# Optimization experiments

Measured on AMD Instinct MI355X. Metric: run time of the kernel, lower is better.

Reference implementation:

```python
import jax, jax.numpy as jnp
import numpy as np

B, S, H, K = 64, 512, 768, 21  # batch, seq_len, bert hidden, num_labels


def setup_inputs() -> dict:
    key = jax.random.key(0)
    ks = jax.random.split(key, 8)
    hidden = jax.random.normal(ks[0], (B, S, H), jnp.float32)  # post-BERT states
    W = jax.random.normal(ks[1], (H, K), jnp.float32) * 0.02    # classifier weight
    b = jnp.zeros((K,), jnp.float32)                            # classifier bias
    start_transitions = jax.random.uniform(ks[2], (K,), jnp.float32, -0.1, 0.1)
    transitions = jax.random.uniform(ks[3], (K, K), jnp.float32, -0.1, 0.1)
    end_transitions = jax.random.uniform(ks[4], (K,), jnp.float32, -0.1, 0.1)
    labels = jax.random.randint(ks[5], (B, S), 0, K)
    # torchcrf requires mask[:, 0] == 1; use variable-length prefix masks
    lengths = jax.random.randint(ks[6], (B,), S // 2, S + 1)
    attention_mask = jnp.arange(S)[None, :] < lengths[:, None]  # [B,S] bool
    return dict(hidden=hidden, W=W, b=b,
                start_transitions=start_transitions,
                transitions=transitions,
                end_transitions=end_transitions,
                labels=labels, attention_mask=attention_mask)


def _crf_nll(logits, labels, mask, start_t, trans, end_t):
    """torchcrf CRF forward (reduction='sum' log-likelihood), negated."""
    fmask = mask.astype(logits.dtype)  # [B,S]
    # ---- numerator: score of the gold path ----
    emit = jnp.take_along_axis(logits, labels[..., None], axis=2)[..., 0]  # [B,S]
    tr = trans[labels[:, :-1], labels[:, 1:]]                              # [B,S-1]
    num = start_t[labels[:, 0]] + emit[:, 0] \
        + jnp.sum((emit[:, 1:] + tr) * fmask[:, 1:], axis=1)
    lengths = mask.sum(axis=1)
    last_tags = jnp.take_along_axis(labels, (lengths - 1)[:, None], axis=1)[:, 0]
    num = num + end_t[last_tags]
    # ---- denominator: forward algorithm (logsumexp recurrence) ----
    alpha0 = start_t[None, :] + logits[:, 0]           # [B,K]
    ems = jnp.swapaxes(logits[:, 1:], 0, 1)            # [S-1,B,K]
    ms = jnp.swapaxes(mask[:, 1:], 0, 1)               # [S-1,B]

    def step(alpha, xs):
        em, m = xs
        nxt = jax.scipy.special.logsumexp(
            alpha[:, :, None] + trans[None, :, :] + em[:, None, :], axis=1)
        return jnp.where(m[:, None], nxt, alpha), None

    alpha, _ = jax.lax.scan(step, alpha0, (ems, ms))
    logZ = jax.scipy.special.logsumexp(alpha + end_t[None, :], axis=1)  # [B]
    return jnp.sum(logZ - num)  # negative log-likelihood (sum over batch)


def reference(hidden, W, b, start_transitions, transitions, end_transitions,
              labels, attention_mask):
    # dropout is identity in eval; the GRU in __init__ is unused in forward
    logits = hidden @ W + b  # [B,S,K]
    nll = _crf_nll(logits, labels, attention_mask,
                   start_transitions, transitions, end_transitions)
    # module returns (logits, -1 * log_likelihood) = (logits, nll)
    return (logits, nll)
```

## Files before the change

### kernel.cpp

```cpp
#include <hip/hip_runtime.h>

#define BSZ 64
#define SEQ 512
#define HID 768
#define NK  21

#define REP21(X) X(0) X(1) X(2) X(3) X(4) X(5) X(6) X(7) X(8) X(9) X(10) \
                 X(11) X(12) X(13) X(14) X(15) X(16) X(17) X(18) X(19) X(20)

__global__ __launch_bounds__(256) void gemm_bias_kernel(
    const float* __restrict__ hidden, const float* __restrict__ W,
    const float* __restrict__ bias, float* __restrict__ out)
{
    __shared__ float hs[128 * 65];
    __shared__ float part[4][64 * NK];

    const int tid  = threadIdx.x;
    const int lane = tid & 63;
    const int wv   = __builtin_amdgcn_readfirstlane(tid >> 6);
    const int cw   = tid & 31;
    const int rr   = tid >> 5;

    const float* gbase = hidden + (size_t)blockIdx.x * 64 * HID;

#define DECL(i) float a##i = 0.f;
    REP21(DECL)
#undef DECL

    for (int ch = 0; ch < 6; ++ch) {
        __syncthreads();
        const float* gsrc = gbase + ch * 128;
        #pragma unroll
        for (int sub = 0; sub < 4; ++sub) {
            const int col = sub * 32 + cw;
            #pragma unroll
            for (int p = 0; p < 8; ++p) {
                const int row = p * 8 + rr;
                hs[col * 65 + row] = gsrc[(size_t)row * HID + col];
            }
        }
        __syncthreads();

        const float* wb   = W + (size_t)(ch * 128 + wv * 32) * NK;
        const float* hcol = hs + (size_t)(wv * 32) * 65 + lane;
        #pragma unroll 4
        for (int cc = 0; cc < 32; ++cc) {
            const float h = hcol[cc * 65];
            const float* w = wb + cc * NK;
#define STEP(i) a##i = fmaf(h, w[i], a##i);
            REP21(STEP)
#undef STEP
        }
    }

    float* pp = &part[wv][lane * NK];
#define ST(i) pp[i] = a##i;
    REP21(ST)
#undef ST
    __syncthreads();

    const int base_out = blockIdx.x * (64 * NK);
    for (int idx = tid; idx < 64 * NK; idx += 256) {
        const int k = idx - (idx / NK) * NK;
        const float s = part[0][idx] + part[1][idx] + part[2][idx] + part[3][idx];
        out[base_out + idx] = s + bias[k];
    }
}

__global__ __launch_bounds__(128) void crf_kernel(
    const float* __restrict__ logits,
    const float* __restrict__ start_t,
    const float* __restrict__ trans,
    const float* __restrict__ end_t,
    const int* __restrict__ labels,
    const int* __restrict__ mask,
    float* __restrict__ per_batch)
{
    __shared__ __align__(16) float Xl[SEQ * NK];
    __shared__ float C[SEQ];
    __shared__ float comb[24];

    const int b    = blockIdx.x;
    const int tid  = threadIdx.x;
    const int lane = tid & 63;
    const int wid  = tid >> 6;

    {
        const float4* g4 = (const float4*)(logits + (size_t)b * SEQ * NK);
        float4* l4 = (float4*)Xl;
        for (int idx = tid; idx < SEQ * NK / 4; idx += 128) l4[idx] = g4[idx];
    }

    const int* lab = labels + b * SEQ;
    const int* msk = mask   + b * SEQ;

    int cnt = 0;
    for (int t = lane; t < SEQ; t += 64) cnt += (msk[t] != 0);
    #pragma unroll
    for (int off = 32; off > 0; off >>= 1) cnt += __shfl_xor(cnt, off, 64);
    const int L = cnt;
    const int m = L >> 1;

    __syncthreads();

    {
        float numacc = 0.f;
        for (int t = tid; t < L; t += 128) {
            if (t == 0) numacc += start_t[lab[0]] + Xl[lab[0]];
            else        numacc += Xl[t * NK + lab[t]] + trans[lab[t - 1] * NK + lab[t]];
        }
        if (tid == 0) numacc += end_t[lab[L - 1]];
        #pragma unroll
        for (int off = 32; off > 0; off >>= 1) numacc += __shfl_xor(numacc, off, 64);
        if (lane == 0) comb[22 + wid] = numacc;
    }

    for (int t = tid; t < SEQ; t += 128) C[t] = Xl[t * NK];
    __syncthreads();

    for (int idx = tid; idx < SEQ * NK; idx += 128) {
        const int t = idx / NK;
        Xl[idx] = __expf(Xl[idx] - C[t]);
    }
    __syncthreads();

    const int jj = (lane < NK) ? lane : NK - 1;

#define RL(v, k) __uint_as_float(__builtin_amdgcn_readlane(__float_as_uint(v), k))

    float a;
    float Orenorm = 0.f;
    float csum = 0.f;

    if (wid == 0) {
        float Ecol[NK];
        #pragma unroll
        for (int k = 0; k < NK; ++k) Ecol[k] = __expf(trans[k * NK + jj]);

        a = __expf(start_t[jj]) * Xl[jj];
        for (int t = lane; t <= m; t += 64) csum += C[t];

        float xv = Xl[NK + jj];
        float xn = Xl[2 * NK + jj];
        for (int t = 1; t <= m; ++t) {
            const float xn2 = Xl[(t + 2) * NK + jj];
            float s0 = RL(a, 0) * Ecol[0];
            float s1 = RL(a, 1) * Ecol[1];
            float s2 = RL(a, 2) * Ecol[2];
            s0 = fmaf(RL(a,  3), Ecol[ 3], s0);
            s1 = fmaf(RL(a,  4), Ecol[ 4], s1);
            s2 = fmaf(RL(a,  5), Ecol[ 5], s2);
            s0 = fmaf(RL(a,  6), Ecol[ 6], s0);
            s1 = fmaf(RL(a,  7), Ecol[ 7], s1);
            s2 = fmaf(RL(a,  8), Ecol[ 8], s2);
            s0 = fmaf(RL(a,  9), Ecol[ 9], s0);
            s1 = fmaf(RL(a, 10), Ecol[10], s1);
            s2 = fmaf(RL(a, 11), Ecol[11], s2);
            s0 = fmaf(RL(a, 12), Ecol[12], s0);
            s1 = fmaf(RL(a, 13), Ecol[13], s1);
            s2 = fmaf(RL(a, 14), Ecol[14], s2);
            s0 = fmaf(RL(a, 15), Ecol[15], s0);
            s1 = fmaf(RL(a, 16), Ecol[16], s1);
            s2 = fmaf(RL(a, 17), Ecol[17], s2);
            s0 = fmaf(RL(a, 18), Ecol[18], s0);
            s1 = fmaf(RL(a, 19), Ecol[19], s1);
            s2 = fmaf(RL(a, 20), Ecol[20], s2);
            a = ((s0 + s1) + s2) * xv;
            if ((t & 7) == 0) {
                const float mm = __uint_as_float(
                    __builtin_amdgcn_readfirstlane(__float_as_uint(a)));
                a *= __builtin_amdgcn_rcpf(mm);
                Orenorm += __logf(mm);
            }
            xv = xn; xn = xn2;
        }
    } else {
        float Erow[NK];
        #pragma unroll
        for (int k = 0; k < NK; ++k) Erow[k] = __expf(trans[jj * NK + k]);

        a = __expf(end_t[jj]);
        for (int t = m + 1 + lane; t < L; t += 64) csum += C[t];

        float xv = Xl[(L - 1) * NK + jj];
        float xn = Xl[max(L - 2, 0) * NK + jj];
        for (int t = L - 1; t > m; --t) {
            const float xn2 = Xl[max(t - 2, 0) * NK + jj];
            const float u = a * xv;
            float s0 = RL(u, 0) * Erow[0];
            float s1 = RL(u, 1) * Erow[1];
            float s2 = RL(u, 2) * Erow[2];
            s0 = fmaf(RL(u,  3), Erow[ 3], s0);
            s1 = fmaf(RL(u,  4), Erow[ 4], s1);
            s2 = fmaf(RL(u,  5), Erow[ 5], s2);
            s0 = fmaf(RL(u,  6), Erow[ 6], s0);
            s1 = fmaf(RL(u,  7), Erow[ 7], s1);
            s2 = fmaf(RL(u,  8), Erow[ 8], s2);
            s0 = fmaf(RL(u,  9), Erow[ 9], s0);
            s1 = fmaf(RL(u, 10), Erow[10], s1);
            s2 = fmaf(RL(u, 11), Erow[11], s2);
            s0 = fmaf(RL(u, 12), Erow[12], s0);
            s1 = fmaf(RL(u, 13), Erow[13], s1);
            s2 = fmaf(RL(u, 14), Erow[14], s2);
            s0 = fmaf(RL(u, 15), Erow[15], s0);
            s1 = fmaf(RL(u, 16), Erow[16], s1);
            s2 = fmaf(RL(u, 17), Erow[17], s2);
            s0 = fmaf(RL(u, 18), Erow[18], s0);
            s1 = fmaf(RL(u, 19), Erow[19], s1);
            s2 = fmaf(RL(u, 20), Erow[20], s2);
            a = (s0 + s1) + s2;
            if ((t & 7) == 0) {
                const float mm = __uint_as_float(
                    __builtin_amdgcn_readfirstlane(__float_as_uint(a)));
                a *= __builtin_amdgcn_rcpf(mm);
                Orenorm += __logf(mm);
            }
            xv = xn; xn = xn2;
        }
    }
#undef RL

    #pragma unroll
    for (int off = 32; off > 0; off >>= 1) csum += __shfl_xor(csum, off, 64);

    if (wid == 1) {
        if (lane < NK) comb[lane] = a;
        if (lane == 0) comb[21] = csum + Orenorm;
    }
    __syncthreads();

    if (wid == 0) {
        float val = (lane < NK) ? a * comb[lane] : 0.f;
        #pragma unroll
        for (int off = 32; off > 0; off >>= 1) val += __shfl_xor(val, off, 64);
        if (lane == 0) {
            const float OF  = csum + Orenorm;
            const float num = comb[22] + comb[23];
            per_batch[b] = OF + comb[21] + __logf(val) - num;
        }
    }
}

__global__ __launch_bounds__(64) void reduce_kernel(
    const float* __restrict__ pb, float* __restrict__ out)
{
    float v = pb[threadIdx.x];
    #pragma unroll
    for (int off = 32; off > 0; off >>= 1) v += __shfl_xor(v, off, 64);
    if (threadIdx.x == 0) out[BSZ * SEQ * NK] = v;
}

extern "C" void kernel_launch(void* const* d_in, const int* in_sizes, int n_in,
                              void* d_out, int out_size, void* d_ws, size_t ws_size,
                              hipStream_t stream)
{
    const float* hidden  = (const float*)d_in[0];
    const float* W       = (const float*)d_in[1];
    const float* bias    = (const float*)d_in[2];
    const float* start_t = (const float*)d_in[3];
    const float* trans   = (const float*)d_in[4];
    const float* end_t   = (const float*)d_in[5];
    const int*   labels  = (const int*)d_in[6];
    const int*   mask    = (const int*)d_in[7];
    float* out = (float*)d_out;
    float* pb  = (float*)d_ws;

    gemm_bias_kernel<<<(BSZ * SEQ) / 64, 256, 0, stream>>>(hidden, W, bias, out);
    crf_kernel<<<BSZ, 128, 0, stream>>>(out, start_t, trans, end_t, labels, mask, pb);
    reduce_kernel<<<1, 64, 0, stream>>>(pb, out);
}
```

Baseline: 250.6 us.

## Double-buffer GEMM hidden tiles via register prefetch and unroll CRF recurrence by eight

Result: faster. 234.4 us (-6.4%).

```diff
diff --git a/kernel.cpp b/kernel.cpp
--- a/kernel.cpp
+++ b/kernel.cpp
@@ -12,7 +12,7 @@
     const float* __restrict__ hidden, const float* __restrict__ W,
     const float* __restrict__ bias, float* __restrict__ out)
 {
-    __shared__ float hs[128 * 65];
+    __shared__ float hs[2][64 * 65];
     __shared__ float part[4][64 * NK];
 
     const int tid  = threadIdx.x;
@@ -27,24 +27,35 @@
     REP21(DECL)
 #undef DECL
 
-    for (int ch = 0; ch < 6; ++ch) {
+    float st[16];
+    #pragma unroll
+    for (int sub = 0; sub < 2; ++sub)
+        #pragma unroll
+        for (int p = 0; p < 8; ++p)
+            st[sub * 8 + p] = gbase[(size_t)(p * 8 + rr) * HID + sub * 32 + cw];
+
+    for (int ch = 0; ch < 12; ++ch) {
+        float* hb = hs[ch & 1];
+        #pragma unroll
+        for (int sub = 0; sub < 2; ++sub)
+            #pragma unroll
+            for (int p = 0; p < 8; ++p)
+                hb[(sub * 32 + cw) * 65 + p * 8 + rr] = st[sub * 8 + p];
         __syncthreads();
-        const float* gsrc = gbase + ch * 128;
-        #pragma unroll
-        for (int sub = 0; sub < 4; ++sub) {
-            const int col = sub * 32 + cw;
+
+        if (ch < 11) {
+            const float* gsrc = gbase + (ch + 1) * 64;
             #pragma unroll
-            for (int p = 0; p < 8; ++p) {
-                const int row = p * 8 + rr;
-                hs[col * 65 + row] = gsrc[(size_t)row * HID + col];
-            }
-        }
-        __syncthreads();
-
-        const float* wb   = W + (size_t)(ch * 128 + wv * 32) * NK;
-        const float* hcol = hs + (size_t)(wv * 32) * 65 + lane;
+            for (int sub = 0; sub < 2; ++sub)
+                #pragma unroll
+                for (int p = 0; p < 8; ++p)
+                    st[sub * 8 + p] = gsrc[(size_t)(p * 8 + rr) * HID + sub * 32 + cw];
+        }
+
+        const float* wb   = W + (size_t)(ch * 64 + wv * 16) * NK;
+        const float* hcol = hb + (size_t)(wv * 16) * 65 + lane;
         #pragma unroll 4
-        for (int cc = 0; cc < 32; ++cc) {
+        for (int cc = 0; cc < 16; ++cc) {
             const float h = hcol[cc * 65];
             const float* w = wb + cc * NK;
 #define STEP(i) a##i = fmaf(h, w[i], a##i);
@@ -127,6 +138,27 @@
     const int jj = (lane < NK) ? lane : NK - 1;
 
 #define RL(v, k) __uint_as_float(__builtin_amdgcn_readlane(__float_as_uint(v), k))
+#define MATVEC(vv, EE, outv) do {                                          \
+    float s0 = RL(vv, 0) * EE[0];                                          \
+    float s1 = RL(vv, 1) * EE[1];                                          \
+    float s2 = RL(vv, 2) * EE[2];                                          \
+    s0 = fmaf(RL(vv,  3), EE[ 3], s0); s1 = fmaf(RL(vv,  4), EE[ 4], s1);  \
+    s2 = fmaf(RL(vv,  5), EE[ 5], s2); s0 = fmaf(RL(vv,  6), EE[ 6], s0);  \
+    s1 = fmaf(RL(vv,  7), EE[ 7], s1); s2 = fmaf(RL(vv,  8), EE[ 8], s2);  \
+    s0 = fmaf(RL(vv,  9), EE[ 9], s0); s1 = fmaf(RL(vv, 10), EE[10], s1);  \
+    s2 = fmaf(RL(vv, 11), EE[11], s2); s0 = fmaf(RL(vv, 12), EE[12], s0);  \
+    s1 = fmaf(RL(vv, 13), EE[13], s1); s2 = fmaf(RL(vv, 14), EE[14], s2);  \
+    s0 = fmaf(RL(vv, 15), EE[15], s0); s1 = fmaf(RL(vv, 16), EE[16], s1);  \
+    s2 = fmaf(RL(vv, 17), EE[17], s2); s0 = fmaf(RL(vv, 18), EE[18], s0);  \
+    s1 = fmaf(RL(vv, 19), EE[19], s1); s2 = fmaf(RL(vv, 20), EE[20], s2);  \
+    outv = (s0 + s1) + s2;                                                 \
+} while (0)
+#define RENORM() do {                                                      \
+    const float mm = __uint_as_float(                                      \
+        __builtin_amdgcn_readfirstlane(__float_as_uint(a)));               \
+    a *= __builtin_amdgcn_rcpf(mm);                                        \
+    Orenorm += __logf(mm);                                                 \
+} while (0)
 
     float a;
     float Orenorm = 0.f;
@@ -140,40 +172,20 @@
         a = __expf(start_t[jj]) * Xl[jj];
         for (int t = lane; t <= m; t += 64) csum += C[t];
 
-        float xv = Xl[NK + jj];
-        float xn = Xl[2 * NK + jj];
-        for (int t = 1; t <= m; ++t) {
-            const float xn2 = Xl[(t + 2) * NK + jj];
-            float s0 = RL(a, 0) * Ecol[0];
-            float s1 = RL(a, 1) * Ecol[1];
-            float s2 = RL(a, 2) * Ecol[2];
-            s0 = fmaf(RL(a,  3), Ecol[ 3], s0);
-            s1 = fmaf(RL(a,  4), Ecol[ 4], s1);
-            s2 = fmaf(RL(a,  5), Ecol[ 5], s2);
-            s0 = fmaf(RL(a,  6), Ecol[ 6], s0);
-            s1 = fmaf(RL(a,  7), Ecol[ 7], s1);
-            s2 = fmaf(RL(a,  8), Ecol[ 8], s2);
-            s0 = fmaf(RL(a,  9), Ecol[ 9], s0);
-            s1 = fmaf(RL(a, 10), Ecol[10], s1);
-            s2 = fmaf(RL(a, 11), Ecol[11], s2);
-            s0 = fmaf(RL(a, 12), Ecol[12], s0);
-            s1 = fmaf(RL(a, 13), Ecol[13], s1);
-            s2 = fmaf(RL(a, 14), Ecol[14], s2);
-            s0 = fmaf(RL(a, 15), Ecol[15], s0);
-            s1 = fmaf(RL(a, 16), Ecol[16], s1);
-            s2 = fmaf(RL(a, 17), Ecol[17], s2);
-            s0 = fmaf(RL(a, 18), Ecol[18], s0);
-            s1 = fmaf(RL(a, 19), Ecol[19], s1);
-            s2 = fmaf(RL(a, 20), Ecol[20], s2);
-            a = ((s0 + s1) + s2) * xv;
-            if ((t & 7) == 0) {
-                const float mm = __uint_as_float(
-                    __builtin_amdgcn_readfirstlane(__float_as_uint(a)));
-                a *= __builtin_amdgcn_rcpf(mm);
-                Orenorm += __logf(mm);
-            }
-            xv = xn; xn = xn2;
-        }
+#define FSTEP(xr) do { float nv; MATVEC(a, Ecol, nv); a = nv * (xr); } while (0)
+        int t0 = 1;
+        for (; t0 + 7 <= m; t0 += 8) {
+            const float* xb = Xl + t0 * NK + jj;
+            const float x0 = xb[0];      const float x1 = xb[NK];
+            const float x2 = xb[2 * NK]; const float x3 = xb[3 * NK];
+            const float x4 = xb[4 * NK]; const float x5 = xb[5 * NK];
+            const float x6 = xb[6 * NK]; const float x7 = xb[7 * NK];
+            FSTEP(x0); FSTEP(x1); FSTEP(x2); FSTEP(x3);
+            FSTEP(x4); FSTEP(x5); FSTEP(x6); FSTEP(x7);
+            RENORM();
+        }
+        for (; t0 <= m; ++t0) { const float x = Xl[t0 * NK + jj]; FSTEP(x); }
+#undef FSTEP
     } else {
         float Erow[NK];
         #pragma unroll
@@ -182,43 +194,24 @@
         a = __expf(end_t[jj]);
         for (int t = m + 1 + lane; t < L; t += 64) csum += C[t];
 
-        float xv = Xl[(L - 1) * NK + jj];
-        float xn = Xl[max(L - 2, 0) * NK + jj];
-        for (int t = L - 1; t > m; --t) {
-            const float xn2 = Xl[max(t - 2, 0) * NK + jj];
-            const float u = a * xv;
-            float s0 = RL(u, 0) * Erow[0];
-            float s1 = RL(u, 1) * Erow[1];
-            float s2 = RL(u, 2) * Erow[2];
-            s0 = fmaf(RL(u,  3), Erow[ 3], s0);
-            s1 = fmaf(RL(u,  4), Erow[ 4], s1);
-            s2 = fmaf(RL(u,  5), Erow[ 5], s2);
-            s0 = fmaf(RL(u,  6), Erow[ 6], s0);
-            s1 = fmaf(RL(u,  7), Erow[ 7], s1);
-            s2 = fmaf(RL(u,  8), Erow[ 8], s2);
-            s0 = fmaf(RL(u,  9), Erow[ 9], s0);
-            s1 = fmaf(RL(u, 10), Erow[10], s1);
-            s2 = fmaf(RL(u, 11), Erow[11], s2);
-            s0 = fmaf(RL(u, 12), Erow[12], s0);
-            s1 = fmaf(RL(u, 13), Erow[13], s1);
-            s2 = fmaf(RL(u, 14), Erow[14], s2);
-            s0 = fmaf(RL(u, 15), Erow[15], s0);
-            s1 = fmaf(RL(u, 16), Erow[16], s1);
-            s2 = fmaf(RL(u, 17), Erow[17], s2);
-            s0 = fmaf(RL(u, 18), Erow[18], s0);
-            s1 = fmaf(RL(u, 19), Erow[19], s1);
-            s2 = fmaf(RL(u, 20), Erow[20], s2);
-            a = (s0 + s1) + s2;
-            if ((t & 7) == 0) {
-                const float mm = __uint_as_float(
-                    __builtin_amdgcn_readfirstlane(__float_as_uint(a)));
-                a *= __builtin_amdgcn_rcpf(mm);
-                Orenorm += __logf(mm);
-            }
-            xv = xn; xn = xn2;
-        }
+#define BSTEP(xr) do { const float u = a * (xr); float nv; MATVEC(u, Erow, nv); a = nv; } while (0)
+        int t0 = L - 1;
+        for (; t0 - 7 >= m + 1; t0 -= 8) {
+            const float* xb = Xl + t0 * NK + jj;
+            const float x0 = xb[0];       const float x1 = xb[-NK];
+            const float x2 = xb[-2 * NK]; const float x3 = xb[-3 * NK];
+            const float x4 = xb[-4 * NK]; const float x5 = xb[-5 * NK];
+            const float x6 = xb[-6 * NK]; const float x7 = xb[-7 * NK];
+            BSTEP(x0); BSTEP(x1); BSTEP(x2); BSTEP(x3);
+            BSTEP(x4); BSTEP(x5); BSTEP(x6); BSTEP(x7);
+            RENORM();
+        }
+        for (; t0 >= m + 1; --t0) { const float x = Xl[t0 * NK + jj]; BSTEP(x); }
+#undef BSTEP
     }
 #undef RL
+#undef MATVEC
+#undef RENORM
 
     #pragma unroll
     for (int off = 32; off > 0; off >>= 1) csum += __shfl_xor(csum, off, 64);
```
